# Kernel optimization log

Measured on AMD Instinct MI355X. Metric: run time of the kernel, lower is better.

The kernel has to match this reference:

```python
import jax, jax.numpy as jnp
import numpy as np

EPS = 1e-12
N_WAY, N_SHOT, C_IN, H_IN, W_IN = 5, 5, 640, 24, 24
TOP_LR = 0.8


def _normalize(x, axis):
    # torch F.normalize: x / max(||x||_2, eps)
    n = jnp.sqrt(jnp.sum(x * x, axis=axis, keepdims=True))
    return x / jnp.maximum(n, EPS)


def _conv1x1(x, W, b):
    # x: (B,C,H,W), W: (O,C), b: (O,)
    return jnp.einsum('bchw,oc->bohw', x, W) + b[None, :, None, None]


def _attlayer(x, Wc, bc, Wq, bq, Wk, bk):
    B, C, H, W = x.shape
    HW = H * W
    n_way, n_shot = N_WAY, N_SHOT
    scale = 1.0 / (C ** 0.5)
    x5 = _conv1x1(x, Wc, bc) + x
    x5 = _conv1x1(x5, Wq, bq)            # note: query_transform applied here
    # query_transform applied AGAIN (faithful to original)
    xq = _conv1x1(x5, Wq, bq).reshape(n_way, n_shot, C, HW)
    x_query = jnp.swapaxes(xq, 2, 3).reshape(n_way, n_shot * HW, C)
    xk = _conv1x1(x5, Wk, bk).reshape(n_way, n_shot, C, HW)
    x_key = jnp.swapaxes(xk, 1, 2).reshape(n_way, C, n_shot * HW)
    x_w1 = jnp.matmul(x_query, x_key) * scale          # (n_way, n_shot*HW, n_shot*HW)
    x_w = x_w1.reshape(n_way, n_shot * HW, n_shot, HW).max(-1).mean(-1)
    x_w = jax.nn.softmax(x_w.reshape(n_way, n_shot, HW), axis=-1)
    norm0 = _normalize(x5, 1).reshape(n_way, n_shot, C, H, W)
    # hard-max mask over spatial positions
    mask = (x_w == x_w.max(-1, keepdims=True)).astype(x.dtype)   # (n_way, n_shot, HW)
    seeds = (norm0 * mask.reshape(n_way, n_shot, 1, H, W)).sum((3, 4))  # (n_way, n_shot, C)
    # conv3d with 1x1 spatial kernel over full channel depth == einsum
    cor = jnp.einsum('nkcyx,okc->noyx', norm0, seeds).reshape(n_way, n_shot, HW)
    cmin = cor.min(-1, keepdims=True)
    cmax = cor.max(-1, keepdims=True)
    cor = (cor - cmin) / (cmax - cmin + EPS)
    cormap = cor.reshape(n_way * n_shot, 1, H, W)
    x51 = (x5 * cormap).reshape(n_way, n_shot, C, H, W)
    return x51.mean((1, 3, 4))  # (n_way, C)


def _cdsnet(lf):
    B, C, H, W = lf.shape
    HW = H * W
    n_way, n_shot = N_WAY, N_SHOT
    lfn = _normalize(lf, 1)
    X = jnp.swapaxes(lfn.reshape(B, C, HW), 1, 2)          # (B, HW, C)
    intra = X.reshape(n_way, n_shot * HW, C)
    # d_intra: masked (1-eye) gram mean == (x_i . S_way - ||x_i||^2)/(n_shot*HW)
    S_way = intra.sum(1)                                    # (n_way, C)
    d_intra = (jnp.einsum('nic,nc->ni', intra, S_way) - (intra * intra).sum(-1)) / (n_shot * HW)
    # d_inter: block-diagonal (same-image) pairs masked out
    S_tot = X.sum((0, 1))                                   # (C,)
    S_img = X.sum(1)                                        # (B, C)
    d_inter = (jnp.einsum('bic,c->bi', X, S_tot) - jnp.einsum('bic,bc->bi', X, S_img)) / (B * HW)
    cds = jax.nn.sigmoid(d_intra.reshape(n_way, -1) / d_inter.reshape(n_way, -1))  # (n_way, n_shot*HW)
    k = int(n_shot * HW * TOP_LR)
    _, sel_idx = jax.lax.top_k(cds, k)
    sel = jnp.zeros((n_way, n_shot * HW), lf.dtype)
    sel = sel.at[jnp.arange(n_way)[:, None], sel_idx].set(1.0)
    pos_small = sel.reshape(n_way * n_shot, 1, H, W)
    slf = lf * pos_small                                    # select_local_features
    slf_n = jnp.swapaxes(_normalize(slf.reshape(B, C, HW), 1), 1, 2)
    slf_n = slf_n.reshape(n_way, n_shot, HW, C)
    m1 = slf_n.reshape(n_way, n_shot * HW, C).mean(1)       # (n_way, C)
    l_intra = jnp.matmul(m1, m1.T) * (1.0 - jnp.eye(n_way, dtype=lf.dtype))
    m2 = slf_n.mean(2)                                      # (n_way, n_shot, C)
    l_inter = jnp.einsum('nsc,ntc->nst', m2, m2) * (1.0 - jnp.eye(n_shot, dtype=lf.dtype))
    loss = jnp.exp(l_inter.mean() / l_intra.mean())
    pos_index = jnp.broadcast_to(pos_small, (B, C, H, W))
    neg_index = 1.0 - pos_index
    return loss, pos_index, neg_index


def setup_inputs() -> dict:
    key = jax.random.key(0)
    ks = jax.random.split(key, 7)
    C = C_IN
    s = N_WAY * N_SHOT
    scale = 1.0 / np.sqrt(C)
    lf = jax.random.normal(ks[0], (s, C, H_IN, W_IN), jnp.float32)
    Wc = jax.random.normal(ks[1], (C, C), jnp.float32) * scale
    bc = jax.random.normal(ks[2], (C,), jnp.float32) * 0.01
    Wq = jax.random.normal(ks[3], (C, C), jnp.float32) * scale
    bq = jax.random.normal(ks[4], (C,), jnp.float32) * 0.01
    Wk = jax.random.normal(ks[5], (C, C), jnp.float32) * scale
    bk = jax.random.normal(ks[6], (C,), jnp.float32) * 0.01
    return {'local_feature': lf, 'Wc': Wc, 'bc': bc, 'Wq': Wq, 'bq': bq, 'Wk': Wk, 'bk': bk}


def reference(local_feature, Wc, bc, Wq, bq, Wk, bk):
    s, c, h, w = local_feature.shape
    hw = h * w
    proto1 = _attlayer(local_feature, Wc, bc, Wq, bq, Wk, bk)   # (n_way, C)
    global_proto = jnp.broadcast_to(proto1[:, None, :], (N_WAY, N_SHOT, c)).reshape(s, c)
    gpa = global_proto[:, None, :]                               # (s, 1, C) -> broadcasts to (s, HW, C)
    contrastive_loss, pos_index, neg_index = _cdsnet(local_feature)
    pos_x = _normalize(jnp.swapaxes((local_feature * pos_index).reshape(s, c, hw), 1, 2), -1)
    neg_x = _normalize(jnp.swapaxes((local_feature * neg_index).reshape(s, c, hw), 1, 2), -1)
    pos_value = jnp.exp(pos_x * gpa).sum(-1).mean(-1).mean(-1)
    neg_value = jnp.exp(neg_x * gpa).sum(-1).mean(-1).mean(-1)
    ctc_loss = -jnp.log(pos_value / neg_value)
    return (contrastive_loss, ctc_loss, pos_index)
```

## Files before the change

kernel.cpp:

```cpp
#include <hip/hip_runtime.h>
#include <math.h>

#define NW 5
#define NS 5
#define BB 25
#define CD 640
#define HWD 576
#define NP 2880
#define KTOP 2304
#define EPSF 1e-12f

typedef __attribute__((ext_vector_type(8))) short short8;
typedef __attribute__((ext_vector_type(4))) float f32x4;

__device__ inline unsigned short f2bf(float x) {
    unsigned u = __float_as_uint(x);
    return (unsigned short)((u + 0x7fffu + ((u >> 16) & 1u)) >> 16);
}
__device__ inline float bf2f(unsigned short h) { return __uint_as_float(((unsigned)h) << 16); }

__device__ inline void gload_lds16(const void* g, void* l) {
    __builtin_amdgcn_global_load_lds(
        (const __attribute__((address_space(1))) unsigned int*)g,
        (__attribute__((address_space(3))) unsigned int*)l, 16, 0, 0);
}

__global__ __launch_bounds__(256) void gemm640(
    const float* __restrict__ A0, const float* __restrict__ B0,
    const float* __restrict__ add0, float* __restrict__ C0, int mode0,
    const float* __restrict__ A1, const float* __restrict__ B1,
    const float* __restrict__ add1, float* __restrict__ C1, int mode1)
{
    __shared__ __align__(16) float At[32][68];
    __shared__ __align__(16) float Bt[32][64];
    const float *A, *B, *add; float* C; int mode;
    if (blockIdx.z == 0) { A = A0; B = B0; add = add0; C = C0; mode = mode0; }
    else                 { A = A1; B = B1; add = add1; C = C1; mode = mode1; }
    const int o0 = blockIdx.y * 64, j0 = blockIdx.x * 64;
    const int t  = threadIdx.x;
    const int to = (t >> 4) * 4, tj = (t & 15) * 4;

    float acc[4][4];
#pragma unroll
    for (int r = 0; r < 4; ++r)
#pragma unroll
        for (int s = 0; s < 4; ++s) acc[r][s] = 0.f;

    for (int c0 = 0; c0 < CD; c0 += 32) {
        __syncthreads();
        {
            const int r = t >> 3, c8 = (t & 7) * 8;
            float4 b0 = *(const float4*)&B[(size_t)(c0+r)*CD + j0 + c8];
            float4 b1 = *(const float4*)&B[(size_t)(c0+r)*CD + j0 + c8 + 4];
            *(float4*)&Bt[r][c8]     = b0;
            *(float4*)&Bt[r][c8 + 4] = b1;
            if (mode == 0) {
                float4 a0 = *(const float4*)&A[(size_t)(c0+r)*CD + o0 + c8];
                float4 a1 = *(const float4*)&A[(size_t)(c0+r)*CD + o0 + c8 + 4];
                *(float4*)&At[r][c8]     = a0;
                *(float4*)&At[r][c8 + 4] = a1;
            } else {
                const int r2 = t >> 2, c82 = (t & 3) * 8;
                float4 a0 = *(const float4*)&A[(size_t)(o0+r2)*CD + c0 + c82];
                float4 a1 = *(const float4*)&A[(size_t)(o0+r2)*CD + c0 + c82 + 4];
                At[c82+0][r2] = a0.x; At[c82+1][r2] = a0.y;
                At[c82+2][r2] = a0.z; At[c82+3][r2] = a0.w;
                At[c82+4][r2] = a1.x; At[c82+5][r2] = a1.y;
                At[c82+6][r2] = a1.z; At[c82+7][r2] = a1.w;
            }
        }
        __syncthreads();
#pragma unroll
        for (int kk = 0; kk < 32; ++kk) {
            float4 av = *(const float4*)&At[kk][to];
            float4 bv = *(const float4*)&Bt[kk][tj];
            float aa[4] = {av.x, av.y, av.z, av.w};
            float bb[4] = {bv.x, bv.y, bv.z, bv.w};
#pragma unroll
            for (int r = 0; r < 4; ++r)
#pragma unroll
                for (int s = 0; s < 4; ++s)
                    acc[r][s] = fmaf(aa[r], bb[s], acc[r][s]);
        }
    }

#pragma unroll
    for (int r = 0; r < 4; ++r) {
        float4 v;
        v.x = acc[r][0]; v.y = acc[r][1]; v.z = acc[r][2]; v.w = acc[r][3];
        if (add != nullptr) {
            float4 ad = *(const float4*)&add[(size_t)(o0+to+r)*CD + j0 + tj];
            v.x += ad.x; v.y += ad.y; v.z += ad.z; v.w += ad.w;
        }
        *(float4*)&C[(size_t)(o0+to+r)*CD + j0 + tj] = v;
    }
}

__global__ void matvec640(const float* __restrict__ A, const float* __restrict__ x,
                          const float* __restrict__ b, float* __restrict__ y)
{
    const int t = threadIdx.x;
    const int o = blockIdx.x*64 + (t >> 2);
    const int cb = (t & 3) * 160;
    const float* ap = A + (size_t)o*CD + cb;
    float a = 0.f;
    for (int m = 0; m < 160; m += 4) {
        float4 v = *(const float4*)&ap[m];
        a = fmaf(v.x, x[cb+m],   a);
        a = fmaf(v.y, x[cb+m+1], a);
        a = fmaf(v.z, x[cb+m+2], a);
        a = fmaf(v.w, x[cb+m+3], a);
    }
    a += __shfl_xor(a, 1, 64); a += __shfl_xor(a, 2, 64);
    if ((t & 3) == 0) y[o] = a + b[o];
}

__global__ void biasvec_kernel(const float* __restrict__ Wq, const float* __restrict__ Wk,
                               const float* __restrict__ bq, const float* __restrict__ bk,
                               float* __restrict__ wqtbk, float* __restrict__ bqwk,
                               float* __restrict__ sbb)
{
    const int c = threadIdx.x;
    const int m0 = blockIdx.x * 160;
    float s1 = 0.f, s2 = 0.f;
    for (int m = m0; m < m0 + 160; ++m) {
        s1 = fmaf(Wq[(size_t)m*CD + c], bk[m], s1);
        s2 = fmaf(bq[m], Wk[(size_t)m*CD + c], s2);
    }
    atomicAdd(&wqtbk[c], s1);
    atomicAdd(&bqwk[c], s2);
    if (c == 0) {
        float s3 = 0.f;
        for (int m = m0; m < m0 + 160; ++m) s3 = fmaf(bq[m], bk[m], s3);
        atomicAdd(sbb, s3);
    }
}

__global__ void wsplit2(const float* __restrict__ Weff, const float* __restrict__ M2e,
                        unsigned short* __restrict__ WeH, unsigned short* __restrict__ WeL,
                        unsigned short* __restrict__ MeH, unsigned short* __restrict__ MeL)
{
    int blk = blockIdx.x;
    const float* S; unsigned short *H, *L;
    if (blk < 400) { S = Weff; H = WeH; L = WeL; }
    else           { S = M2e;  H = MeH; L = MeL; blk -= 400; }
    int i = blk*256 + threadIdx.x;
    float4 v = ((const float4*)S)[i];
    ushort4 h, l;
    h.x = f2bf(v.x); h.y = f2bf(v.y); h.z = f2bf(v.z); h.w = f2bf(v.w);
    l.x = f2bf(v.x - bf2f(h.x)); l.y = f2bf(v.y - bf2f(h.y));
    l.z = f2bf(v.z - bf2f(h.z)); l.w = f2bf(v.w - bf2f(h.w));
    ((ushort4*)H)[i] = h; ((ushort4*)L)[i] = l;
}

__global__ __launch_bounds__(256) void convert_t(const float* __restrict__ in,
        unsigned short* __restrict__ Oh, unsigned short* __restrict__ Ol)
{
    __shared__ float tile[64][65];
    const int b  = blockIdx.y;
    const int c0 = (blockIdx.x / 9) * 64;
    const int p0 = (blockIdx.x % 9) * 64;
    const int t  = threadIdx.x;
    const float* src = in + (size_t)b * CD * HWD;
#pragma unroll
    for (int it = 0; it < 4; ++it) {
        int cl = (t >> 4) + 16*it, pl = (t & 15) * 4;
        float4 v = *(const float4*)&src[(size_t)(c0+cl)*HWD + p0 + pl];
        tile[cl][pl] = v.x; tile[cl][pl+1] = v.y; tile[cl][pl+2] = v.z; tile[cl][pl+3] = v.w;
    }
    __syncthreads();
#pragma unroll
    for (int it = 0; it < 4; ++it) {
        int pl = (t >> 4) + 16*it, clb = (t & 15) * 4;
        ushort4 hv, lv;
        float x0 = tile[clb+0][pl], x1 = tile[clb+1][pl], x2 = tile[clb+2][pl], x3 = tile[clb+3][pl];
        hv.x = f2bf(x0); hv.y = f2bf(x1); hv.z = f2bf(x2); hv.w = f2bf(x3);
        lv.x = f2bf(x0 - bf2f(hv.x)); lv.y = f2bf(x1 - bf2f(hv.y));
        lv.z = f2bf(x2 - bf2f(hv.z)); lv.w = f2bf(x3 - bf2f(hv.w));
        size_t o = (size_t)(b*HWD + p0 + pl) * CD + c0 + clb;
        *(ushort4*)&Oh[o] = hv;
        *(ushort4*)&Ol[o] = lv;
    }
}

__global__ __launch_bounds__(256) void conv2x(
    const unsigned short* __restrict__ Ah_, const unsigned short* __restrict__ Al_,
    const unsigned short* __restrict__ WeH, const unsigned short* __restrict__ WeL,
    const unsigned short* __restrict__ MeH, const unsigned short* __restrict__ MeL,
    const float* __restrict__ beff, const float* __restrict__ wbias,
    unsigned short* __restrict__ x5h, unsigned short* __restrict__ x5l,
    unsigned short* __restrict__ wh,  unsigned short* __restrict__ wl)
{
    __shared__ __align__(16) unsigned short lds[14336];
    const int obx  = blockIdx.x;
    const int osel = (obx < 5);
    const int o0   = (osel ? obx : obx - 5) * 128;
    const unsigned short* Wh = osel ? WeH : MeH;
    const unsigned short* Wl = osel ? WeL : MeL;
    const float* bias = osel ? beff : wbias;
    unsigned short* Oh = osel ? x5h : wh;
    unsigned short* Ol = osel ? x5l : wl;
    const int row0 = blockIdx.y * 96;
    const int t    = threadIdx.x;
    const int w    = t >> 6, lane = t & 63;
    const int ihalf = (w & 1) * 48;
    const int jhalf = (w >> 1) * 64;

    f32x4 acc[3][4];
#pragma unroll
    for (int f = 0; f < 3; ++f)
#pragma unroll
        for (int g = 0; g < 4; ++g) acc[f][g] = (f32x4){0.f,0.f,0.f,0.f};

    const int rl = lane >> 2;
    const int cl = (lane & 3) * 8;

    for (int c0 = 0; c0 < CD; c0 += 32) {
#pragma unroll
        for (int e = 0; e < 7; ++e) {
            const int s = w*7 + e;
            const unsigned short* src;
            if (s < 6)        src = Ah_ + (size_t)(row0 + s*16      + rl)*CD + c0 + cl;
            else if (s < 12)  src = Al_ + (size_t)(row0 + (s-6)*16  + rl)*CD + c0 + cl;
            else if (s < 20)  src = Wh  + (size_t)(o0   + (s-12)*16 + rl)*CD + c0 + cl;
            else              src = Wl  + (size_t)(o0   + (s-20)*16 + rl)*CD + c0 + cl;
            gload_lds16(src, &lds[s*512]);
        }
        __syncthreads();

        const int chunk = (lane >> 4) * 8;
        short8 afh[3], afl[3];
#pragma unroll
        for (int f = 0; f < 3; ++f) {
            int row = ihalf + f*16 + (lane & 15);
            afh[f] = *(const short8*)&lds[row*32 + chunk];
            afl[f] = *(const short8*)&lds[3072 + row*32 + chunk];
        }
#pragma unroll
        for (int g = 0; g < 4; ++g) {
            int row = jhalf + g*16 + (lane & 15);
            short8 bfh = *(const short8*)&lds[6144  + row*32 + chunk];
            short8 bfl = *(const short8*)&lds[10240 + row*32 + chunk];
#pragma unroll
            for (int f = 0; f < 3; ++f) {
                acc[f][g] = __builtin_amdgcn_mfma_f32_16x16x32_bf16(afh[f], bfh, acc[f][g], 0, 0, 0);
                acc[f][g] = __builtin_amdgcn_mfma_f32_16x16x32_bf16(afh[f], bfl, acc[f][g], 0, 0, 0);
                acc[f][g] = __builtin_amdgcn_mfma_f32_16x16x32_bf16(afl[f], bfh, acc[f][g], 0, 0, 0);
            }
        }
        __syncthreads();
    }

#pragma unroll
    for (int g = 0; g < 4; ++g) {
        const int o = o0 + jhalf + g*16 + (lane & 15);
        const float bs = bias[o];
#pragma unroll
        for (int f = 0; f < 3; ++f) {
            const int rbase = row0 + ihalf + f*16 + (lane >> 4)*4;
#pragma unroll
            for (int r = 0; r < 4; ++r) {
                const size_t idx = (size_t)(rbase + r)*CD + o;
                float v = acc[f][g][r] + bs;
                unsigned short hi = f2bf(v);
                Oh[idx] = hi;
                Ol[idx] = f2bf(v - bf2f(hi));
            }
        }
    }
}

__global__ __launch_bounds__(256) void qk_mfma(
    const unsigned short* __restrict__ Qh, const unsigned short* __restrict__ Ql,
    const unsigned short* __restrict__ Kh, const unsigned short* __restrict__ Kl,
    const float* __restrict__ rvec, float* __restrict__ xwp)
{
    __shared__ __align__(16) unsigned short lds[18432];
    const int n    = blockIdx.z;
    const int i0   = blockIdx.x * 96;
    const int shot = blockIdx.y / 3;
    const int jt   = blockIdx.y % 3;
    const int t    = threadIdx.x;
    const int w    = t >> 6, lane = t & 63;
    const int ihalf = (w & 1) * 48;
    const int jhalf = (w >> 1) * 96;

    const size_t qbase = (size_t)(n*NP + i0) * CD;
    const size_t kbase = (size_t)(n*NP + shot*HWD + jt*192) * CD;

    f32x4 acc[3][6];
#pragma unroll
    for (int f = 0; f < 3; ++f)
#pragma unroll
        for (int g = 0; g < 6; ++g) acc[f][g] = (f32x4){0.f,0.f,0.f,0.f};

    const int rl = lane >> 2;
    const int cl = (lane & 3) * 8;

    for (int c0 = 0; c0 < CD; c0 += 32) {
#pragma unroll
        for (int e = 0; e < 9; ++e) {
            const int s = w*9 + e;
            const int r = s*16 + rl;
            const unsigned short* src;
            if (s < 6)        src = Qh + qbase + (size_t)r*CD        + c0 + cl;
            else if (s < 12)  src = Ql + qbase + (size_t)(r-96)*CD   + c0 + cl;
            else if (s < 24)  src = Kh + kbase + (size_t)(r-192)*CD  + c0 + cl;
            else              src = Kl + kbase + (size_t)(r-384)*CD  + c0 + cl;
            gload_lds16(src, &lds[s*512]);
        }
        __syncthreads();

        const int chunk = (lane >> 4) * 8;
        short8 afh[3], afl[3];
#pragma unroll
        for (int f = 0; f < 3; ++f) {
            int row = ihalf + f*16 + (lane & 15);
            afh[f] = *(const short8*)&lds[row*32 + chunk];
            afl[f] = *(const short8*)&lds[3072 + row*32 + chunk];
        }
#pragma unroll
        for (int g = 0; g < 6; ++g) {
            int row = jhalf + g*16 + (lane & 15);
            short8 bfh = *(const short8*)&lds[6144  + row*32 + chunk];
            short8 bfl = *(const short8*)&lds[12288 + row*32 + chunk];
#pragma unroll
            for (int f = 0; f < 3; ++f) {
                acc[f][g] = __builtin_amdgcn_mfma_f32_16x16x32_bf16(afh[f], bfh, acc[f][g], 0, 0, 0);
                acc[f][g] = __builtin_amdgcn_mfma_f32_16x16x32_bf16(afh[f], bfl, acc[f][g], 0, 0, 0);
                acc[f][g] = __builtin_amdgcn_mfma_f32_16x16x32_bf16(afl[f], bfh, acc[f][g], 0, 0, 0);
            }
        }
        __syncthreads();
    }

    float rv[6];
    {
        int jg0 = n*NP + shot*HWD + jt*192 + jhalf + (lane & 15);
#pragma unroll
        for (int g = 0; g < 6; ++g) rv[g] = rvec[jg0 + g*16];
    }
    float* smax = (float*)lds;
#pragma unroll
    for (int f = 0; f < 3; ++f) {
#pragma unroll
        for (int r = 0; r < 4; ++r) {
            float m = -INFINITY;
#pragma unroll
            for (int g = 0; g < 6; ++g) m = fmaxf(m, acc[f][g][r] + rv[g]);
#pragma unroll
            for (int off = 1; off < 16; off <<= 1) m = fmaxf(m, __shfl_xor(m, off, 64));
            if ((lane & 15) == 0) smax[(ihalf + f*16 + (lane >> 4)*4 + r)*2 + (w >> 1)] = m;
        }
    }
    __syncthreads();
    if (t < 96) {
        float m = fmaxf(smax[t*2], smax[t*2 + 1]);
        xwp[(((size_t)n*5 + shot)*3 + jt)*NP + i0 + t] = m;
    }
}

__global__ void argmax_seeds(const float* __restrict__ xwp,
        const unsigned short* __restrict__ Xh, const unsigned short* __restrict__ Xl,
        const float* __restrict__ invn5, float* __restrict__ seeds)
{
    const int b = blockIdx.x;
    const int n = b / NS, sq = b % NS;
    const int t = threadIdx.x;
    __shared__ float wv[9]; __shared__ int wi[9]; __shared__ int spix;
    if (t < 576) {
        const int i = sq * HWD + t;
        float v = 0.f;
#pragma unroll
        for (int s = 0; s < NS; ++s) {
            float m = -INFINITY;
#pragma unroll
            for (int tt = 0; tt < 3; ++tt)
                m = fmaxf(m, xwp[(((size_t)(n*NS+s))*3 + tt)*NP + i]);
            v += m;
        }
        int lane = t & 63, w = t >> 6;
        float bv = v; int bi = t;
        for (int off = 32; off; off >>= 1) {
            float ov = __shfl_down(bv, off, 64);
            int   oi = __shfl_down(bi, off, 64);
            if (ov > bv || (ov == bv && oi < bi)) { bv = ov; bi = oi; }
        }
        if (lane == 0) { wv[w] = bv; wi[w] = bi; }
    }
    __syncthreads();
    if (t == 0) {
        float best = wv[0]; int bidx = wi[0];
        for (int k = 1; k < 9; ++k)
            if (wv[k] > best || (wv[k] == best && wi[k] < bidx)) { best = wv[k]; bidx = wi[k]; }
        spix = bidx;
    }
    __syncthreads();
    const int row = b*HWD + spix;
    float v = bf2f(Xh[(size_t)row*CD + t]) + bf2f(Xl[(size_t)row*CD + t]);
    seeds[b*CD + t] = v * invn5[row];
}

__global__ __launch_bounds__(256) void norms_rvec_T(const unsigned short* __restrict__ Xh,
        const unsigned short* __restrict__ Xl, const float* __restrict__ bqwk,
        const float* __restrict__ sbb, float* __restrict__ invn, float* __restrict__ rvec)
{
    const int t = threadIdx.x;
    const int row = blockIdx.x*64 + (t >> 2);
    const int cb = (t & 3) * 160;
    const unsigned short* ph = Xh + (size_t)row*CD + cb;
    const unsigned short* pl = Xl + (size_t)row*CD + cb;
    const float* wv = bqwk + cb;
    float a = 0.f, d = 0.f;
    for (int c = 0; c < 160; c += 8) {
        short8 h8 = *(const short8*)&ph[c];
        short8 l8 = *(const short8*)&pl[c];
#pragma unroll
        for (int j = 0; j < 8; ++j) {
            float v = bf2f((unsigned short)h8[j]) + bf2f((unsigned short)l8[j]);
            a = fmaf(v, v, a);
            d = fmaf(v, wv[c+j], d);
        }
    }
    a += __shfl_xor(a, 1, 64); a += __shfl_xor(a, 2, 64);
    d += __shfl_xor(d, 1, 64); d += __shfl_xor(d, 2, 64);
    if ((t & 3) == 0) {
        invn[row] = 1.f / fmaxf(sqrtf(a), EPSF);
        rvec[row] = d + sbb[0];
    }
}

__global__ __launch_bounds__(256) void pixel_norms(const float* __restrict__ src, float* __restrict__ invn)
{
    const int b = blockIdx.y, t = threadIdx.x;
    const int p = blockIdx.x*64 + (t >> 2);
    const int cb = (t & 3) * 160;
    const float* sp = src + (size_t)b*CD*HWD + p + (size_t)cb*HWD;
    float a = 0.f;
    for (int c = 0; c < 160; ++c) { float v = sp[(size_t)c*HWD]; a = fmaf(v, v, a); }
    a += __shfl_xor(a, 1, 64); a += __shfl_xor(a, 2, 64);
    if ((t & 3) == 0) invn[b*HWD + p] = 1.f / fmaxf(sqrtf(a), EPSF);
}

__global__ __launch_bounds__(256) void cor_T(const unsigned short* __restrict__ Xh,
        const unsigned short* __restrict__ Xl, const float* __restrict__ invn5,
        const float* __restrict__ seeds, float* __restrict__ cor)
{
    const int b = blockIdx.y;
    const int n = b / NS, k = b % NS;
    const int t = threadIdx.x;
    const int p = blockIdx.x*64 + (t >> 2);
    const int row = b*HWD + p;
    const int cb = (t & 3) * 160;
    const unsigned short* ph = Xh + (size_t)row*CD + cb;
    const unsigned short* pl = Xl + (size_t)row*CD + cb;
    float a[5] = {0.f,0.f,0.f,0.f,0.f};
    for (int c = 0; c < 160; c += 8) {
        short8 h8 = *(const short8*)&ph[c];
        short8 l8 = *(const short8*)&pl[c];
#pragma unroll
        for (int j = 0; j < 8; ++j) {
            float v = bf2f((unsigned short)h8[j]) + bf2f((unsigned short)l8[j]);
#pragma unroll
            for (int o = 0; o < 5; ++o)
                a[o] = fmaf(v, seeds[(o*NS + k)*CD + cb + c + j], a[o]);
        }
    }
    float in1 = invn5[row];
#pragma unroll
    for (int o = 0; o < 5; ++o) {
        float s = a[o];
        s += __shfl_xor(s, 1, 64); s += __shfl_xor(s, 2, 64);
        if ((t & 3) == 0) atomicAdd(&cor[(n*5 + o)*HWD + p], in1 * s);
    }
}

__global__ __launch_bounds__(256) void proto1_nm(const unsigned short* __restrict__ Xh,
        const unsigned short* __restrict__ Xl, const float* __restrict__ cor,
        float* __restrict__ proto1)
{
    __shared__ float corb[NP];
    __shared__ float sacc[256];
    __shared__ float mnv[5], mxv[5];
    const int n = blockIdx.y;
    const int t = threadIdx.x;
    for (int j = t; j < NP; j += 256) corb[j] = cor[n*NP + j];
    __syncthreads();
    if (t < 320) {
        int o = t >> 6, lane = t & 63;
        float mn = INFINITY, mx = -INFINITY;
        for (int j = lane; j < HWD; j += 64) {
            float v = corb[o*HWD + j];
            mn = fminf(mn, v); mx = fmaxf(mx, v);
        }
        for (int off = 32; off; off >>= 1) {
            mn = fminf(mn, __shfl_xor(mn, off, 64));
            mx = fmaxf(mx, __shfl_xor(mx, off, 64));
        }
        if (lane == 0) { mnv[o] = mn; mxv[o] = mx; }
    }
    __syncthreads();
    for (int j = t; j < NP; j += 256) {
        int o = j / HWD;
        corb[j] = (corb[j] - mnv[o]) / (mxv[o] - mnv[o] + EPSF);
    }
    __syncthreads();
    const int c = blockIdx.x*64 + (t & 63);
    const int rc = t >> 6;
    float a = 0.f;
    for (int rr = rc*720; rr < rc*720 + 720; ++rr) {
        size_t row = (size_t)(n*NP + rr);
        float v = bf2f(Xh[row*CD + c]) + bf2f(Xl[row*CD + c]);
        a = fmaf(v, corb[rr], a);
    }
    sacc[t] = a;
    __syncthreads();
    if (t < 64) {
        float s = sacc[t] + sacc[t+64] + sacc[t+128] + sacc[t+192];
        proto1[n*CD + c] = s * (1.f / 2880.f);
    }
}

__global__ void masked_sum(const float* __restrict__ lf, const float* __restrict__ invn,
                           const float* __restrict__ mask, float* __restrict__ out)
{
    int b = blockIdx.y; int ct = blockIdx.x;
    int t = threadIdx.x; int pi = t & 63, cj = t >> 6;
    int c = ct * 4 + cj;
    const float* xp = lf + ((size_t)b * CD + c) * HWD;
    const float* ip = invn + b * HWD;
    float acc = 0.f;
    if (mask != nullptr) {
        const float* mp = mask + b * HWD;
        for (int p = pi; p < HWD; p += 64) acc = fmaf(xp[p], ip[p] * mp[p], acc);
    } else {
        for (int p = pi; p < HWD; p += 64) acc = fmaf(xp[p], ip[p], acc);
    }
    for (int off = 32; off; off >>= 1) acc += __shfl_down(acc, off, 64);
    if (pi == 0) out[b * CD + c] = acc;
}

__global__ void sway_stot(const float* __restrict__ S_img, float* __restrict__ S_way,
                          float* __restrict__ S_tot)
{
    int c = threadIdx.x;
    float tot = 0.f;
    for (int nn = 0; nn < NW; ++nn) {
        float w = 0.f;
        for (int s = 0; s < NS; ++s) w += S_img[(nn*NS+s)*CD + c];
        S_way[nn*CD + c] = w; tot += w;
    }
    S_tot[c] = tot;
}

__global__ __launch_bounds__(256) void cds_v2(const float* __restrict__ lf, const float* __restrict__ invn,
                           const float* __restrict__ S_way, const float* __restrict__ S_img,
                           const float* __restrict__ S_tot, float* __restrict__ cds)
{
    const int b = blockIdx.y, t = threadIdx.x;
    const int p = blockIdx.x*64 + (t >> 2);
    const int cb = (t & 3) * 160;
    const int n = b / NS;
    const float* xp = lf + (size_t)b*CD*HWD + p + (size_t)cb*HWD;
    const float* wv = S_way + n*CD + cb;
    const float* iv = S_img + b*CD + cb;
    const float* tv = S_tot + cb;
    float dw = 0.f, di = 0.f, dt = 0.f, sq = 0.f;
    for (int c = 0; c < 160; ++c) {
        float v = xp[(size_t)c*HWD];
        dw = fmaf(v, wv[c], dw);
        di = fmaf(v, iv[c], di);
        dt = fmaf(v, tv[c], dt);
        sq = fmaf(v, v, sq);
    }
    dw += __shfl_xor(dw,1,64); dw += __shfl_xor(dw,2,64);
    di += __shfl_xor(di,1,64); di += __shfl_xor(di,2,64);
    dt += __shfl_xor(dt,1,64); dt += __shfl_xor(dt,2,64);
    sq += __shfl_xor(sq,1,64); sq += __shfl_xor(sq,2,64);
    if ((t & 3) == 0) {
        float in1 = invn[b*HWD + p];
        float d_intra = (in1 * dw - in1 * in1 * sq) * (1.f / 2880.f);
        float d_inter = (in1 * dt - in1 * di) * (1.f / 14400.f);
        float r = d_intra / d_inter;
        cds[n * NP + (b % NS) * HWD + p] = 1.f / (1.f + expf(-r));
    }
}

__global__ void topk_kernel(const float* __restrict__ cds, float* __restrict__ sel)
{
    __shared__ unsigned int u[NP];
    __shared__ int hist[256];
    __shared__ int red[16];
    __shared__ int bcast;
    __shared__ unsigned sprefix;
    __shared__ int skk;
    __shared__ int scanbuf[576];
    const int n = blockIdx.x, t = threadIdx.x;
    for (int j = t; j < NP; j += 576) {
        unsigned int x = __float_as_uint(cds[n * NP + j]);
        u[j] = (x & 0x80000000u) ? ~x : (x | 0x80000000u);
    }
    if (t == 0) { skk = KTOP; sprefix = 0u; }
    __syncthreads();
    const int j0 = t * 5;
    for (int byte = 3; byte >= 0; --byte) {
        if (t < 256) hist[t] = 0;
        __syncthreads();
        const int sh = byte * 8;
        const unsigned pmask = (byte == 3) ? 0u : (0xFFFFFFFFu << (sh + 8));
        const unsigned pref = sprefix;
#pragma unroll
        for (int e = 0; e < 5; ++e) {
            unsigned v = u[j0+e];
            if ((v & pmask) == pref) atomicAdd(&hist[(v >> sh) & 255], 1);
        }
        __syncthreads();
        if (t == 0) {
            int kk = skk, acc = 0, b2;
            for (b2 = 255; b2 >= 0; --b2) { acc += hist[b2]; if (acc >= kk) break; }
            skk = kk - (acc - hist[b2]);
            sprefix = pref | ((unsigned)b2 << sh);
        }
        __syncthreads();
    }
    const unsigned int T = sprefix;
    int cg = 0, ce = 0;
#pragma unroll
    for (int e = 0; e < 5; ++e) {
        unsigned v = u[j0+e];
        if (v > T) cg++; else if (v == T) ce++;
    }
    const int lane = t & 63, w = t >> 6;
    int r1 = cg;
    for (int off = 32; off; off >>= 1) r1 += __shfl_down(r1, off, 64);
    if (lane == 0) red[w] = r1;
    __syncthreads();
    if (t == 0) { int s2 = 0; for (int q = 0; q < 9; ++q) s2 += red[q]; bcast = s2; }
    __syncthreads();
    const int need = KTOP - bcast;
    scanbuf[t] = ce;
    __syncthreads();
    for (int off = 1; off < 576; off <<= 1) {
        int v2 = (t >= off) ? scanbuf[t - off] : 0;
        __syncthreads();
        scanbuf[t] += v2;
        __syncthreads();
    }
    int excl = scanbuf[t] - ce;
    int eidx = 0;
#pragma unroll
    for (int e = 0; e < 5; ++e) {
        int j = j0 + e;
        unsigned v = u[j];
        float s = 0.f;
        if (v > T) s = 1.f;
        else if (v == T) { if (excl + eidx < need) s = 1.f; eidx++; }
        int sh2 = j / HWD;
        sel[(n*NS + sh2) * HWD + (j - sh2*HWD)] = s;
    }
}

__global__ __launch_bounds__(256) void ctc_v2(const float* __restrict__ lf, const float* __restrict__ invn,
                           const float* __restrict__ proto1, const float* __restrict__ sel,
                           float* __restrict__ scal)
{
    const int b = blockIdx.y, t = threadIdx.x;
    const int p = blockIdx.x*64 + (t >> 2);
    const int cb = (t & 3) * 160;
    const int n = b / NS;
    const float* xp = lf + (size_t)b*CD*HWD + p + (size_t)cb*HWD;
    const float* pr = proto1 + n*CD + cb;
    float in1 = invn[b*HWD + p];
    float acc = 0.f;
    for (int c = 0; c < 160; ++c) acc += expf(xp[(size_t)c*HWD] * in1 * pr[c]);
    acc += __shfl_xor(acc, 1, 64); acc += __shfl_xor(acc, 2, 64);
    float pv = 0.f, nv = 0.f;
    if ((t & 3) == 0) {
        float s = sel[b*HWD + p];
        pv = (s > 0.5f) ? acc : 640.f;
        nv = (s > 0.5f) ? 640.f : acc;
    }
    for (int off = 32; off >= 4; off >>= 1) {
        pv += __shfl_down(pv, off, 64);
        nv += __shfl_down(nv, off, 64);
    }
    if ((t & 63) == 0) { atomicAdd(&scal[0], pv); atomicAdd(&scal[1], nv); }
}

__global__ void closs_fin(const float* __restrict__ Sm, const float* __restrict__ scal,
                          float* __restrict__ out)
{
    if (blockIdx.x == 1) {
        if (threadIdx.x == 0) out[1] = -(logf(scal[0]) - logf(scal[1]));
        return;
    }
    int c = threadIdx.x;
    double A = 0.0, Bv = 0.0, Cv = 0.0;
    float tot = 0.f;
    for (int nn = 0; nn < NW; ++nn) {
        float ws = 0.f;
        for (int s = 0; s < NS; ++s) {
            float v = Sm[(nn*NS+s)*CD + c];
            ws += v; Cv += (double)v * v;
        }
        tot += ws; A += (double)ws * ws;
    }
    Bv = (double)tot * tot;
    int lane = c & 63, w = c >> 6;
    for (int off = 32; off; off >>= 1) {
        A  += __shfl_down(A,  off, 64);
        Bv += __shfl_down(Bv, off, 64);
        Cv += __shfl_down(Cv, off, 64);
    }
    __shared__ double sa[10], sb[10], sc[10];
    if (lane == 0) { sa[w] = A; sb[w] = Bv; sc[w] = Cv; }
    __syncthreads();
    if (c == 0) {
        double a = 0, b2 = 0, cc = 0;
        for (int q = 0; q < 10; ++q) { a += sa[q]; b2 += sb[q]; cc += sc[q]; }
        out[0] = (float)exp(5.0 * (a - cc) / (b2 - a));
    }
}

__global__ void posindex_kernel(const float* __restrict__ sel, float* __restrict__ out2)
{
    int idx = blockIdx.x * 256 + threadIdx.x;
    int row = idx / 144;
    int f4  = idx - row * 144;
    int b   = row / CD;
    const float* sp = sel + b * HWD + f4 * 4;
    float* op = out2 + (size_t)row * HWD + f4 * 4;
    float2 v0 = make_float2(sp[0], sp[1]);
    float2 v1 = make_float2(sp[2], sp[3]);
    *(float2*)op = v0; *(float2*)(op + 2) = v1;
}

__global__ void init_zero(float* __restrict__ cor, float* __restrict__ scal,
                          float* __restrict__ wqtbk, float* __restrict__ bqwk,
                          float* __restrict__ sbb)
{
    int i = blockIdx.x * 256 + threadIdx.x;
    if (i < BB * HWD) cor[i] = 0.f;
    if (i < 640) { wqtbk[i] = 0.f; bqwk[i] = 0.f; }
    if (i < 2) scal[i] = 0.f;
    if (i == 0) sbb[0] = 0.f;
}

extern "C" void kernel_launch(void* const* d_in, const int* in_sizes, int n_in,
                              void* d_out, int out_size, void* d_ws, size_t ws_size,
                              hipStream_t stream) {
    const float* lf = (const float*)d_in[0];
    const float* Wc = (const float*)d_in[1];
    const float* bc = (const float*)d_in[2];
    const float* Wq = (const float*)d_in[3];
    const float* bq = (const float*)d_in[4];
    const float* Wk = (const float*)d_in[5];
    const float* bk = (const float*)d_in[6];
    float* out = (float*)d_out;
    float* ws = (float*)d_ws;

    const size_t FEAT = 9216000;
    size_t off = 0;
    auto alloc = [&](size_t nf) { float* p = ws + off; off += (nf + 3) & ~(size_t)3; return p; };
    float* s0     = alloc(FEAT);
    float* s1     = alloc(FEAT);
    float* xwp    = alloc(216000);
    float* seeds  = alloc(16000);
    float* invn5  = alloc(14400);
    float* invnl  = alloc(14400);
    float* cor    = alloc(14400);
    float* proto1 = alloc(3200);
    float* S_img  = alloc(16000);
    float* S_way  = alloc(3200);
    float* S_tot  = alloc(640);
    float* cds    = alloc(14400);
    float* sel    = alloc(14400);
    float* Sm     = alloc(16000);
    float* scal   = alloc(8);
    float* wqtbk  = alloc(640);
    float* bqwk   = alloc(640);
    float* sbb    = alloc(4);
    float* rvec   = alloc(14400);
    float* beff   = alloc(640);
    float* wbias  = alloc(640);
    float* WeS    = alloc(409600);
    float* MeS    = alloc(409600);

    float* M2   = s1;
    float* Weff = s1 + 409600;
    float* M2e  = s1 + 819200;

    unsigned short* WeH = (unsigned short*)WeS; unsigned short* WeL = WeH + 409600;
    unsigned short* MeH = (unsigned short*)MeS; unsigned short* MeL = MeH + 409600;

    unsigned short* lfTh = (unsigned short*)(out + 2);
    unsigned short* lfTl = lfTh + FEAT;

    unsigned short* s0h = (unsigned short*)s0; unsigned short* s0l = s0h + FEAT;
    unsigned short* s1h = (unsigned short*)s1; unsigned short* s1l = s1h + FEAT;

    init_zero<<<57, 256, 0, stream>>>(cor, scal, wqtbk, bqwk, sbb);
    gemm640<<<dim3(10,10,2), 256, 0, stream>>>(Wq, Wk, nullptr, M2, 0,
                                               Wq, Wc, Wq,      Weff, 1);
    biasvec_kernel<<<4, 640, 0, stream>>>(Wq, Wk, bq, bk, wqtbk, bqwk, sbb);
    gemm640<<<dim3(10,10,1), 256, 0, stream>>>(M2, Weff, nullptr, M2e, 1,
                                               M2, Weff, nullptr, M2e, 1);
    matvec640<<<10, 256, 0, stream>>>(Wq, bc, bq, beff);
    matvec640<<<10, 256, 0, stream>>>(M2, beff, wqtbk, wbias);
    wsplit2<<<800, 256, 0, stream>>>(Weff, M2e, WeH, WeL, MeH, MeL);

    convert_t<<<dim3(90,25), 256, 0, stream>>>(lf, lfTh, lfTl);

    conv2x<<<dim3(10,150), 256, 0, stream>>>(lfTh, lfTl, WeH, WeL, MeH, MeL,
                                             beff, wbias, s0h, s0l, s1h, s1l);

    norms_rvec_T<<<225, 256, 0, stream>>>(s0h, s0l, bqwk, sbb, invn5, rvec);

    qk_mfma<<<dim3(30,15,5), 256, 0, stream>>>(s0h, s0l, s1h, s1l, rvec, xwp);

    pixel_norms<<<dim3(9,25), 256, 0, stream>>>(lf, invnl);
    argmax_seeds<<<25, 640, 0, stream>>>(xwp, s0h, s0l, invn5, seeds);
    cor_T<<<dim3(9,25), 256, 0, stream>>>(s0h, s0l, invn5, seeds, cor);
    proto1_nm<<<dim3(10,5), 256, 0, stream>>>(s0h, s0l, cor, proto1);

    masked_sum<<<dim3(160,25), 256, 0, stream>>>(lf, invnl, nullptr, S_img);
    sway_stot<<<1, 640, 0, stream>>>(S_img, S_way, S_tot);
    cds_v2<<<dim3(9,25), 256, 0, stream>>>(lf, invnl, S_way, S_img, S_tot, cds);
    topk_kernel<<<5, 576, 0, stream>>>(cds, sel);
    masked_sum<<<dim3(160,25), 256, 0, stream>>>(lf, invnl, sel, Sm);

    ctc_v2<<<dim3(9,25), 256, 0, stream>>>(lf, invnl, proto1, sel, scal);
    closs_fin<<<2, 640, 0, stream>>>(Sm, scal, out);

    posindex_kernel<<<9000, 256, 0, stream>>>(sel, out + 2);
}
```

Measured before the change: 771.3 us.

## Merge independent kernels into multi-role launches and fuse row norms into conv epilogue

Independent kernels are merged into fewer launches, each dispatching on block index: weight GEMMs, bias matvecs, input conversion and zeroing run together in one launch, and post-processing stages are grouped into four launches. The M2e GEMM now writes its bf16 hi/lo split directly, so the fp32 intermediate and a separate split pass are gone. Row sum-of-squares and the bias dot product are accumulated inside the conv epilogue with shuffles and atomics, which removes the separate norms pass over the bf16 features. The intent is to cut launch overhead and redundant memory traffic. In exchange, the conv epilogue gets extra work and atomics, and the merged launches mix block types with uneven cost.

```diff
diff --git a/kernel.cpp b/kernel.cpp
--- a/kernel.cpp
+++ b/kernel.cpp
@@ -25,18 +25,14 @@
         (__attribute__((address_space(3))) unsigned int*)l, 16, 0, 0);
 }
 
-__global__ __launch_bounds__(256) void gemm640(
-    const float* __restrict__ A0, const float* __restrict__ B0,
-    const float* __restrict__ add0, float* __restrict__ C0, int mode0,
-    const float* __restrict__ A1, const float* __restrict__ B1,
-    const float* __restrict__ add1, float* __restrict__ C1, int mode1)
-{
-    __shared__ __align__(16) float At[32][68];
-    __shared__ __align__(16) float Bt[32][64];
-    const float *A, *B, *add; float* C; int mode;
-    if (blockIdx.z == 0) { A = A0; B = B0; add = add0; C = C0; mode = mode0; }
-    else                 { A = A1; B = B1; add = add1; C = C1; mode = mode1; }
-    const int o0 = blockIdx.y * 64, j0 = blockIdx.x * 64;
+__device__ void dev_gemm640(const float* __restrict__ A, const float* __restrict__ B,
+                            const float* __restrict__ add, float* __restrict__ C,
+                            unsigned short* __restrict__ H, unsigned short* __restrict__ L,
+                            int mode, int bx, int by, char* smem)
+{
+    float (*At)[68] = (float(*)[68])smem;
+    float (*Bt)[64] = (float(*)[64])(smem + 8704);
+    const int o0 = by * 64, j0 = bx * 64;
     const int t  = threadIdx.x;
     const int to = (t >> 4) * 4, tj = (t & 15) * 4;
 
@@ -86,80 +82,32 @@
 
 #pragma unroll
     for (int r = 0; r < 4; ++r) {
-        float4 v;
-        v.x = acc[r][0]; v.y = acc[r][1]; v.z = acc[r][2]; v.w = acc[r][3];
+        float v[4] = {acc[r][0], acc[r][1], acc[r][2], acc[r][3]};
+        const size_t base = (size_t)(o0+to+r)*CD + j0 + tj;
         if (add != nullptr) {
-            float4 ad = *(const float4*)&add[(size_t)(o0+to+r)*CD + j0 + tj];
-            v.x += ad.x; v.y += ad.y; v.z += ad.z; v.w += ad.w;
-        }
-        *(float4*)&C[(size_t)(o0+to+r)*CD + j0 + tj] = v;
-    }
-}
-
-__global__ void matvec640(const float* __restrict__ A, const float* __restrict__ x,
-                          const float* __restrict__ b, float* __restrict__ y)
-{
-    const int t = threadIdx.x;
-    const int o = blockIdx.x*64 + (t >> 2);
-    const int cb = (t & 3) * 160;
-    const float* ap = A + (size_t)o*CD + cb;
-    float a = 0.f;
-    for (int m = 0; m < 160; m += 4) {
-        float4 v = *(const float4*)&ap[m];
-        a = fmaf(v.x, x[cb+m],   a);
-        a = fmaf(v.y, x[cb+m+1], a);
-        a = fmaf(v.z, x[cb+m+2], a);
-        a = fmaf(v.w, x[cb+m+3], a);
-    }
-    a += __shfl_xor(a, 1, 64); a += __shfl_xor(a, 2, 64);
-    if ((t & 3) == 0) y[o] = a + b[o];
-}
-
-__global__ void biasvec_kernel(const float* __restrict__ Wq, const float* __restrict__ Wk,
-                               const float* __restrict__ bq, const float* __restrict__ bk,
-                               float* __restrict__ wqtbk, float* __restrict__ bqwk,
-                               float* __restrict__ sbb)
-{
-    const int c = threadIdx.x;
-    const int m0 = blockIdx.x * 160;
-    float s1 = 0.f, s2 = 0.f;
-    for (int m = m0; m < m0 + 160; ++m) {
-        s1 = fmaf(Wq[(size_t)m*CD + c], bk[m], s1);
-        s2 = fmaf(bq[m], Wk[(size_t)m*CD + c], s2);
-    }
-    atomicAdd(&wqtbk[c], s1);
-    atomicAdd(&bqwk[c], s2);
-    if (c == 0) {
-        float s3 = 0.f;
-        for (int m = m0; m < m0 + 160; ++m) s3 = fmaf(bq[m], bk[m], s3);
-        atomicAdd(sbb, s3);
-    }
-}
-
-__global__ void wsplit2(const float* __restrict__ Weff, const float* __restrict__ M2e,
-                        unsigned short* __restrict__ WeH, unsigned short* __restrict__ WeL,
-                        unsigned short* __restrict__ MeH, unsigned short* __restrict__ MeL)
-{
-    int blk = blockIdx.x;
-    const float* S; unsigned short *H, *L;
-    if (blk < 400) { S = Weff; H = WeH; L = WeL; }
-    else           { S = M2e;  H = MeH; L = MeL; blk -= 400; }
-    int i = blk*256 + threadIdx.x;
-    float4 v = ((const float4*)S)[i];
-    ushort4 h, l;
-    h.x = f2bf(v.x); h.y = f2bf(v.y); h.z = f2bf(v.z); h.w = f2bf(v.w);
-    l.x = f2bf(v.x - bf2f(h.x)); l.y = f2bf(v.y - bf2f(h.y));
-    l.z = f2bf(v.z - bf2f(h.z)); l.w = f2bf(v.w - bf2f(h.w));
-    ((ushort4*)H)[i] = h; ((ushort4*)L)[i] = l;
-}
-
-__global__ __launch_bounds__(256) void convert_t(const float* __restrict__ in,
-        unsigned short* __restrict__ Oh, unsigned short* __restrict__ Ol)
-{
-    __shared__ float tile[64][65];
-    const int b  = blockIdx.y;
-    const int c0 = (blockIdx.x / 9) * 64;
-    const int p0 = (blockIdx.x % 9) * 64;
+            float4 ad = *(const float4*)&add[base];
+            v[0] += ad.x; v[1] += ad.y; v[2] += ad.z; v[3] += ad.w;
+        }
+        if (C != nullptr) {
+            float4 o4; o4.x = v[0]; o4.y = v[1]; o4.z = v[2]; o4.w = v[3];
+            *(float4*)&C[base] = o4;
+        }
+        if (H != nullptr) {
+            ushort4 h, l;
+            h.x = f2bf(v[0]); h.y = f2bf(v[1]); h.z = f2bf(v[2]); h.w = f2bf(v[3]);
+            l.x = f2bf(v[0] - bf2f(h.x)); l.y = f2bf(v[1] - bf2f(h.y));
+            l.z = f2bf(v[2] - bf2f(h.z)); l.w = f2bf(v[3] - bf2f(h.w));
+            *(ushort4*)&H[base] = h; *(ushort4*)&L[base] = l;
+        }
+    }
+}
+
+__device__ void dev_convert(const float* __restrict__ in, unsigned short* __restrict__ Oh,
+                            unsigned short* __restrict__ Ol, int b, int xidx, char* smem)
+{
+    float (*tile)[65] = (float(*)[65])smem;
+    const int c0 = (xidx / 9) * 64;
+    const int p0 = (xidx % 9) * 64;
     const int t  = threadIdx.x;
     const float* src = in + (size_t)b * CD * HWD;
 #pragma unroll
@@ -183,13 +131,104 @@
     }
 }
 
+__global__ __launch_bounds__(256) void prep_a(
+    const float* __restrict__ lf, const float* __restrict__ Wc,
+    const float* __restrict__ bc, const float* __restrict__ Wq,
+    const float* __restrict__ bq, const float* __restrict__ Wk,
+    const float* __restrict__ bk,
+    float* __restrict__ M2, float* __restrict__ Weff,
+    float* __restrict__ wqtbk, float* __restrict__ bqwk, float* __restrict__ beff,
+    float* __restrict__ sbb,
+    unsigned short* __restrict__ lfTh, unsigned short* __restrict__ lfTl,
+    float* __restrict__ cor, float* __restrict__ sumsq, float* __restrict__ rvsum,
+    float* __restrict__ proto1, float* __restrict__ scal)
+{
+    __shared__ __align__(16) char smem[16896];
+    const int blk = blockIdx.x;
+    const int t = threadIdx.x;
+    if (blk < 100) {
+        dev_gemm640(Wq, Wk, nullptr, M2, nullptr, nullptr, 0, blk % 10, blk / 10, smem);
+    } else if (blk < 200) {
+        int b2 = blk - 100;
+        dev_gemm640(Wq, Wc, Wq, Weff, nullptr, nullptr, 1, b2 % 10, b2 / 10, smem);
+    } else if (blk < 210) {
+        const int o = (blk - 200)*64 + (t >> 2);
+        const int m0 = (t & 3) * 160;
+        float s1 = 0.f, s2 = 0.f;
+        for (int m = m0; m < m0 + 160; ++m) {
+            s1 = fmaf(Wq[(size_t)m*CD + o], bk[m], s1);
+            s2 = fmaf(bq[m], Wk[(size_t)m*CD + o], s2);
+        }
+        s1 += __shfl_xor(s1, 1, 64); s1 += __shfl_xor(s1, 2, 64);
+        s2 += __shfl_xor(s2, 1, 64); s2 += __shfl_xor(s2, 2, 64);
+        if ((t & 3) == 0) { wqtbk[o] = s1; bqwk[o] = s2; }
+    } else if (blk < 220) {
+        const int o = (blk - 210)*64 + (t >> 2);
+        const int m0 = (t & 3) * 160;
+        const float* ap = Wq + (size_t)o*CD + m0;
+        float a = 0.f;
+        for (int m = 0; m < 160; ++m) a = fmaf(ap[m], bc[m0 + m], a);
+        a += __shfl_xor(a, 1, 64); a += __shfl_xor(a, 2, 64);
+        if ((t & 3) == 0) beff[o] = a + bq[o];
+    } else if (blk == 220) {
+        __shared__ float red[4];
+        float a = 0.f;
+        for (int m = t; m < CD; m += 256) a = fmaf(bq[m], bk[m], a);
+        for (int off2 = 32; off2; off2 >>= 1) a += __shfl_down(a, off2, 64);
+        if ((t & 63) == 0) red[t >> 6] = a;
+        __syncthreads();
+        if (t == 0) sbb[0] = red[0] + red[1] + red[2] + red[3];
+    } else if (blk < 2471) {
+        const int idx = blk - 221;
+        dev_convert(lf, lfTh, lfTl, idx / 90, idx % 90, smem);
+    } else {
+        const int i0 = (blk - 2471)*256 + t;
+        for (int i = i0; i < 14400; i += 8192) { cor[i] = 0.f; sumsq[i] = 0.f; rvsum[i] = 0.f; }
+        for (int i = i0; i < 3200; i += 8192) proto1[i] = 0.f;
+        if (i0 < 2) scal[i0] = 0.f;
+    }
+}
+
+__global__ __launch_bounds__(256) void prep_b(
+    const float* __restrict__ M2, const float* __restrict__ Weff,
+    const float* __restrict__ beff, const float* __restrict__ wqtbk,
+    unsigned short* __restrict__ WeH, unsigned short* __restrict__ WeL,
+    unsigned short* __restrict__ MeH, unsigned short* __restrict__ MeL,
+    float* __restrict__ wbias)
+{
+    __shared__ __align__(16) char smem[16896];
+    const int blk = blockIdx.x;
+    const int t = threadIdx.x;
+    if (blk < 100) {
+        dev_gemm640(M2, Weff, nullptr, nullptr, MeH, MeL, 1, blk % 10, blk / 10, smem);
+    } else if (blk < 200) {
+        int i = (blk - 100)*256 + t;
+        float4 v = ((const float4*)Weff)[i];
+        ushort4 h, l;
+        h.x = f2bf(v.x); h.y = f2bf(v.y); h.z = f2bf(v.z); h.w = f2bf(v.w);
+        l.x = f2bf(v.x - bf2f(h.x)); l.y = f2bf(v.y - bf2f(h.y));
+        l.z = f2bf(v.z - bf2f(h.z)); l.w = f2bf(v.w - bf2f(h.w));
+        ((ushort4*)WeH)[i] = h; ((ushort4*)WeL)[i] = l;
+    } else {
+        const int o = (blk - 200)*64 + (t >> 2);
+        const int m0 = (t & 3) * 160;
+        const float* ap = M2 + (size_t)o*CD + m0;
+        float a = 0.f;
+        for (int m = 0; m < 160; ++m) a = fmaf(ap[m], beff[m0 + m], a);
+        a += __shfl_xor(a, 1, 64); a += __shfl_xor(a, 2, 64);
+        if ((t & 3) == 0) wbias[o] = a + wqtbk[o];
+    }
+}
+
 __global__ __launch_bounds__(256) void conv2x(
     const unsigned short* __restrict__ Ah_, const unsigned short* __restrict__ Al_,
     const unsigned short* __restrict__ WeH, const unsigned short* __restrict__ WeL,
     const unsigned short* __restrict__ MeH, const unsigned short* __restrict__ MeL,
     const float* __restrict__ beff, const float* __restrict__ wbias,
+    const float* __restrict__ bqwk,
     unsigned short* __restrict__ x5h, unsigned short* __restrict__ x5l,
-    unsigned short* __restrict__ wh,  unsigned short* __restrict__ wl)
+    unsigned short* __restrict__ wh,  unsigned short* __restrict__ wl,
+    float* __restrict__ sumsq, float* __restrict__ rvsum)
 {
     __shared__ __align__(16) unsigned short lds[14336];
     const int obx  = blockIdx.x;
@@ -251,20 +290,39 @@
         __syncthreads();
     }
 
+    float bs[4], bw[4];
 #pragma unroll
     for (int g = 0; g < 4; ++g) {
         const int o = o0 + jhalf + g*16 + (lane & 15);
-        const float bs = bias[o];
-#pragma unroll
-        for (int f = 0; f < 3; ++f) {
-            const int rbase = row0 + ihalf + f*16 + (lane >> 4)*4;
-#pragma unroll
-            for (int r = 0; r < 4; ++r) {
+        bs[g] = bias[o];
+        bw[g] = osel ? bqwk[o] : 0.f;
+    }
+#pragma unroll
+    for (int f = 0; f < 3; ++f) {
+        const int rbase = row0 + ihalf + f*16 + (lane >> 4)*4;
+#pragma unroll
+        for (int r = 0; r < 4; ++r) {
+            float sq = 0.f, rv = 0.f;
+#pragma unroll
+            for (int g = 0; g < 4; ++g) {
+                const int o = o0 + jhalf + g*16 + (lane & 15);
                 const size_t idx = (size_t)(rbase + r)*CD + o;
-                float v = acc[f][g][r] + bs;
+                float v = acc[f][g][r] + bs[g];
                 unsigned short hi = f2bf(v);
                 Oh[idx] = hi;
                 Ol[idx] = f2bf(v - bf2f(hi));
+                sq = fmaf(v, v, sq);
+                rv = fmaf(v, bw[g], rv);
+            }
+            if (osel) {
+                sq += __shfl_xor(sq, 1, 64); rv += __shfl_xor(rv, 1, 64);
+                sq += __shfl_xor(sq, 2, 64); rv += __shfl_xor(rv, 2, 64);
+                sq += __shfl_xor(sq, 4, 64); rv += __shfl_xor(rv, 4, 64);
+                sq += __shfl_xor(sq, 8, 64); rv += __shfl_xor(rv, 8, 64);
+                if ((lane & 15) == 0) {
+                    atomicAdd(&sumsq[rbase + r], sq);
+                    atomicAdd(&rvsum[rbase + r], rv);
+                }
             }
         }
     }
@@ -273,7 +331,8 @@
 __global__ __launch_bounds__(256) void qk_mfma(
     const unsigned short* __restrict__ Qh, const unsigned short* __restrict__ Ql,
     const unsigned short* __restrict__ Kh, const unsigned short* __restrict__ Kl,
-    const float* __restrict__ rvec, float* __restrict__ xwp)
+    const float* __restrict__ rvsum, const float* __restrict__ sbb,
+    float* __restrict__ xwp)
 {
     __shared__ __align__(16) unsigned short lds[18432];
     const int n    = blockIdx.z;
@@ -334,11 +393,12 @@
         __syncthreads();
     }
 
+    const float sv = sbb[0];
     float rv[6];
     {
         int jg0 = n*NP + shot*HWD + jt*192 + jhalf + (lane & 15);
 #pragma unroll
-        for (int g = 0; g < 6; ++g) rv[g] = rvec[jg0 + g*16];
+        for (int g = 0; g < 6; ++g) rv[g] = rvsum[jg0 + g*16] + sv;
     }
     float* smax = (float*)lds;
 #pragma unroll
@@ -360,13 +420,27 @@
     }
 }
 
-__global__ void argmax_seeds(const float* __restrict__ xwp,
-        const unsigned short* __restrict__ Xh, const unsigned short* __restrict__ Xl,
-        const float* __restrict__ invn5, float* __restrict__ seeds)
-{
-    const int b = blockIdx.x;
+__global__ __launch_bounds__(640) void post_a(
+    const float* __restrict__ lf, const float* __restrict__ xwp,
+    const unsigned short* __restrict__ Xh, const unsigned short* __restrict__ Xl,
+    const float* __restrict__ sumsq, float* __restrict__ invnl,
+    float* __restrict__ seeds)
+{
+    const int blk = blockIdx.x;
+    const int t = threadIdx.x;
+    if (blk < 90) {
+        const int pg = blk*160 + (t >> 2);
+        const int cb = (t & 3) * 160;
+        const int b = pg / HWD, p = pg - (pg / HWD) * HWD;
+        const float* sp = lf + (size_t)b*CD*HWD + (size_t)cb*HWD + p;
+        float a = 0.f;
+        for (int c = 0; c < 160; ++c) { float v = sp[(size_t)c*HWD]; a = fmaf(v, v, a); }
+        a += __shfl_xor(a, 1, 64); a += __shfl_xor(a, 2, 64);
+        if ((t & 3) == 0) invnl[pg] = 1.f / fmaxf(sqrtf(a), EPSF);
+        return;
+    }
+    const int b = blk - 90;
     const int n = b / NS, sq = b % NS;
-    const int t = threadIdx.x;
     __shared__ float wv[9]; __shared__ int wi[9]; __shared__ int spix;
     if (t < 576) {
         const int i = sq * HWD + t;
@@ -397,160 +471,123 @@
     }
     __syncthreads();
     const int row = b*HWD + spix;
+    const float in1 = 1.f / fmaxf(sqrtf(sumsq[row]), EPSF);
     float v = bf2f(Xh[(size_t)row*CD + t]) + bf2f(Xl[(size_t)row*CD + t]);
-    seeds[b*CD + t] = v * invn5[row];
-}
-
-__global__ __launch_bounds__(256) void norms_rvec_T(const unsigned short* __restrict__ Xh,
-        const unsigned short* __restrict__ Xl, const float* __restrict__ bqwk,
-        const float* __restrict__ sbb, float* __restrict__ invn, float* __restrict__ rvec)
-{
+    seeds[b*CD + t] = v * in1;
+}
+
+__global__ __launch_bounds__(256) void post_b(
+    const unsigned short* __restrict__ Xh, const unsigned short* __restrict__ Xl,
+    const float* __restrict__ sumsq, const float* __restrict__ seeds,
+    const float* __restrict__ lf, const float* __restrict__ invnl,
+    float* __restrict__ cor, float* __restrict__ S_img)
+{
+    const int blk = blockIdx.x;
     const int t = threadIdx.x;
-    const int row = blockIdx.x*64 + (t >> 2);
-    const int cb = (t & 3) * 160;
-    const unsigned short* ph = Xh + (size_t)row*CD + cb;
-    const unsigned short* pl = Xl + (size_t)row*CD + cb;
-    const float* wv = bqwk + cb;
-    float a = 0.f, d = 0.f;
-    for (int c = 0; c < 160; c += 8) {
-        short8 h8 = *(const short8*)&ph[c];
-        short8 l8 = *(const short8*)&pl[c];
-#pragma unroll
-        for (int j = 0; j < 8; ++j) {
-            float v = bf2f((unsigned short)h8[j]) + bf2f((unsigned short)l8[j]);
-            a = fmaf(v, v, a);
-            d = fmaf(v, wv[c+j], d);
-        }
-    }
-    a += __shfl_xor(a, 1, 64); a += __shfl_xor(a, 2, 64);
-    d += __shfl_xor(d, 1, 64); d += __shfl_xor(d, 2, 64);
-    if ((t & 3) == 0) {
-        invn[row] = 1.f / fmaxf(sqrtf(a), EPSF);
-        rvec[row] = d + sbb[0];
-    }
-}
-
-__global__ __launch_bounds__(256) void pixel_norms(const float* __restrict__ src, float* __restrict__ invn)
-{
-    const int b = blockIdx.y, t = threadIdx.x;
-    const int p = blockIdx.x*64 + (t >> 2);
-    const int cb = (t & 3) * 160;
-    const float* sp = src + (size_t)b*CD*HWD + p + (size_t)cb*HWD;
-    float a = 0.f;
-    for (int c = 0; c < 160; ++c) { float v = sp[(size_t)c*HWD]; a = fmaf(v, v, a); }
-    a += __shfl_xor(a, 1, 64); a += __shfl_xor(a, 2, 64);
-    if ((t & 3) == 0) invn[b*HWD + p] = 1.f / fmaxf(sqrtf(a), EPSF);
-}
-
-__global__ __launch_bounds__(256) void cor_T(const unsigned short* __restrict__ Xh,
-        const unsigned short* __restrict__ Xl, const float* __restrict__ invn5,
-        const float* __restrict__ seeds, float* __restrict__ cor)
-{
-    const int b = blockIdx.y;
-    const int n = b / NS, k = b % NS;
+    if (blk < 900) {
+        const int zc = blk / 225, rem = blk % 225;
+        const int pb = rem % 9, b = rem / 9;
+        const int n = b / NS, k = b % NS;
+        const int p = pb*64 + (t >> 2);
+        const int row = b*HWD + p;
+        const int cb = zc*160 + (t & 3) * 40;
+        const unsigned short* ph = Xh + (size_t)row*CD + cb;
+        const unsigned short* pl = Xl + (size_t)row*CD + cb;
+        float a[5] = {0.f,0.f,0.f,0.f,0.f};
+        for (int c = 0; c < 40; c += 8) {
+            short8 h8 = *(const short8*)&ph[c];
+            short8 l8 = *(const short8*)&pl[c];
+#pragma unroll
+            for (int j = 0; j < 8; ++j) {
+                float v = bf2f((unsigned short)h8[j]) + bf2f((unsigned short)l8[j]);
+#pragma unroll
+                for (int o = 0; o < 5; ++o)
+                    a[o] = fmaf(v, seeds[(o*NS + k)*CD + cb + c + j], a[o]);
+            }
+        }
+        const float in1 = 1.f / fmaxf(sqrtf(sumsq[row]), EPSF);
+#pragma unroll
+        for (int o = 0; o < 5; ++o) {
+            float s = a[o];
+            s += __shfl_xor(s, 1, 64); s += __shfl_xor(s, 2, 64);
+            if ((t & 3) == 0) atomicAdd(&cor[(n*5 + o)*HWD + p], in1 * s);
+        }
+        return;
+    }
+    const int i = blk - 900;
+    const int ct = i % 160, b = i / 160;
+    const int pi = t & 63, cj = t >> 6;
+    const int c = ct * 4 + cj;
+    const float* xp = lf + ((size_t)b * CD + c) * HWD;
+    const float* ip = invnl + b * HWD;
+    float acc = 0.f;
+    for (int p = pi; p < HWD; p += 64) acc = fmaf(xp[p], ip[p], acc);
+    for (int off = 32; off; off >>= 1) acc += __shfl_down(acc, off, 64);
+    if (pi == 0) S_img[b * CD + c] = acc;
+}
+
+__global__ __launch_bounds__(256) void post_c(
+    const unsigned short* __restrict__ Xh, const unsigned short* __restrict__ Xl,
+    const float* __restrict__ cor, const float* __restrict__ S_img,
+    float* __restrict__ proto1, float* __restrict__ S_way, float* __restrict__ S_tot)
+{
+    const int blk = blockIdx.x;
     const int t = threadIdx.x;
-    const int p = blockIdx.x*64 + (t >> 2);
-    const int row = b*HWD + p;
-    const int cb = (t & 3) * 160;
-    const unsigned short* ph = Xh + (size_t)row*CD + cb;
-    const unsigned short* pl = Xl + (size_t)row*CD + cb;
-    float a[5] = {0.f,0.f,0.f,0.f,0.f};
-    for (int c = 0; c < 160; c += 8) {
-        short8 h8 = *(const short8*)&ph[c];
-        short8 l8 = *(const short8*)&pl[c];
-#pragma unroll
-        for (int j = 0; j < 8; ++j) {
-            float v = bf2f((unsigned short)h8[j]) + bf2f((unsigned short)l8[j]);
-#pragma unroll
-            for (int o = 0; o < 5; ++o)
-                a[o] = fmaf(v, seeds[(o*NS + k)*CD + cb + c + j], a[o]);
-        }
-    }
-    float in1 = invn5[row];
-#pragma unroll
-    for (int o = 0; o < 5; ++o) {
-        float s = a[o];
-        s += __shfl_xor(s, 1, 64); s += __shfl_xor(s, 2, 64);
-        if ((t & 3) == 0) atomicAdd(&cor[(n*5 + o)*HWD + p], in1 * s);
-    }
-}
-
-__global__ __launch_bounds__(256) void proto1_nm(const unsigned short* __restrict__ Xh,
-        const unsigned short* __restrict__ Xl, const float* __restrict__ cor,
-        float* __restrict__ proto1)
-{
-    __shared__ float corb[NP];
-    __shared__ float sacc[256];
-    __shared__ float mnv[5], mxv[5];
-    const int n = blockIdx.y;
-    const int t = threadIdx.x;
-    for (int j = t; j < NP; j += 256) corb[j] = cor[n*NP + j];
-    __syncthreads();
-    if (t < 320) {
-        int o = t >> 6, lane = t & 63;
-        float mn = INFINITY, mx = -INFINITY;
-        for (int j = lane; j < HWD; j += 64) {
-            float v = corb[o*HWD + j];
-            mn = fminf(mn, v); mx = fmaxf(mx, v);
-        }
-        for (int off = 32; off; off >>= 1) {
-            mn = fminf(mn, __shfl_xor(mn, off, 64));
-            mx = fmaxf(mx, __shfl_xor(mx, off, 64));
-        }
-        if (lane == 0) { mnv[o] = mn; mxv[o] = mx; }
-    }
-    __syncthreads();
-    for (int j = t; j < NP; j += 256) {
-        int o = j / HWD;
-        corb[j] = (corb[j] - mnv[o]) / (mxv[o] - mnv[o] + EPSF);
-    }
-    __syncthreads();
-    const int c = blockIdx.x*64 + (t & 63);
-    const int rc = t >> 6;
-    float a = 0.f;
-    for (int rr = rc*720; rr < rc*720 + 720; ++rr) {
-        size_t row = (size_t)(n*NP + rr);
-        float v = bf2f(Xh[row*CD + c]) + bf2f(Xl[row*CD + c]);
-        a = fmaf(v, corb[rr], a);
-    }
-    sacc[t] = a;
-    __syncthreads();
-    if (t < 64) {
-        float s = sacc[t] + sacc[t+64] + sacc[t+128] + sacc[t+192];
-        proto1[n*CD + c] = s * (1.f / 2880.f);
-    }
-}
-
-__global__ void masked_sum(const float* __restrict__ lf, const float* __restrict__ invn,
-                           const float* __restrict__ mask, float* __restrict__ out)
-{
-    int b = blockIdx.y; int ct = blockIdx.x;
-    int t = threadIdx.x; int pi = t & 63, cj = t >> 6;
-    int c = ct * 4 + cj;
-    const float* xp = lf + ((size_t)b * CD + c) * HWD;
-    const float* ip = invn + b * HWD;
-    float acc = 0.f;
-    if (mask != nullptr) {
-        const float* mp = mask + b * HWD;
-        for (int p = pi; p < HWD; p += 64) acc = fmaf(xp[p], ip[p] * mp[p], acc);
-    } else {
-        for (int p = pi; p < HWD; p += 64) acc = fmaf(xp[p], ip[p], acc);
-    }
-    for (int off = 32; off; off >>= 1) acc += __shfl_down(acc, off, 64);
-    if (pi == 0) out[b * CD + c] = acc;
-}
-
-__global__ void sway_stot(const float* __restrict__ S_img, float* __restrict__ S_way,
-                          float* __restrict__ S_tot)
-{
-    int c = threadIdx.x;
-    float tot = 0.f;
-    for (int nn = 0; nn < NW; ++nn) {
-        float w = 0.f;
-        for (int s = 0; s < NS; ++s) w += S_img[(nn*NS+s)*CD + c];
-        S_way[nn*CD + c] = w; tot += w;
-    }
-    S_tot[c] = tot;
+    if (blk < 200) {
+        __shared__ float corb[NP];
+        __shared__ float sacc[256];
+        __shared__ float mnv[5], mxv[5];
+        const int n = blk / 40, rem = blk % 40;
+        const int ct = rem % 10, rch = rem / 10;
+        for (int j = t; j < NP; j += 256) corb[j] = cor[n*NP + j];
+        __syncthreads();
+        {
+            const int lane = t & 63;
+            for (int o = t >> 6; o < 5; o += 4) {
+                float mn = INFINITY, mx = -INFINITY;
+                for (int j = lane; j < HWD; j += 64) {
+                    float v = corb[o*HWD + j];
+                    mn = fminf(mn, v); mx = fmaxf(mx, v);
+                }
+                for (int off = 32; off; off >>= 1) {
+                    mn = fminf(mn, __shfl_xor(mn, off, 64));
+                    mx = fmaxf(mx, __shfl_xor(mx, off, 64));
+                }
+                if (lane == 0) { mnv[o] = mn; mxv[o] = mx; }
+            }
+        }
+        __syncthreads();
+        for (int j = t; j < NP; j += 256) {
+            int o = j / HWD;
+            corb[j] = (corb[j] - mnv[o]) / (mxv[o] - mnv[o] + EPSF);
+        }
+        __syncthreads();
+        const int c = ct*64 + (t & 63);
+        const int rc = t >> 6;
+        const int r0 = rch*720 + rc*180;
+        float a = 0.f;
+        for (int rr = r0; rr < r0 + 180; ++rr) {
+            size_t row = (size_t)(n*NP + rr);
+            float v = bf2f(Xh[row*CD + c]) + bf2f(Xl[row*CD + c]);
+            a = fmaf(v, corb[rr], a);
+        }
+        sacc[t] = a;
+        __syncthreads();
+        if (t < 64) {
+            float s = sacc[t] + sacc[t+64] + sacc[t+128] + sacc[t+192];
+            atomicAdd(&proto1[n*CD + c], s * (1.f / 2880.f));
+        }
+        return;
+    }
+    for (int c = t; c < CD; c += 256) {
+        float tot = 0.f;
+        for (int nn = 0; nn < NW; ++nn) {
+            float w = 0.f;
+            for (int s = 0; s < NS; ++s) w += S_img[(nn*NS+s)*CD + c];
+            S_way[nn*CD + c] = w; tot += w;
+        }
+        S_tot[c] = tot;
+    }
 }
 
 __global__ __launch_bounds__(256) void cds_v2(const float* __restrict__ lf, const float* __restrict__ invn,
@@ -660,17 +697,34 @@
     }
 }
 
-__global__ __launch_bounds__(256) void ctc_v2(const float* __restrict__ lf, const float* __restrict__ invn,
-                           const float* __restrict__ proto1, const float* __restrict__ sel,
-                           float* __restrict__ scal)
-{
-    const int b = blockIdx.y, t = threadIdx.x;
-    const int p = blockIdx.x*64 + (t >> 2);
+__global__ __launch_bounds__(256) void post_d(
+    const float* __restrict__ lf, const float* __restrict__ invnl,
+    const float* __restrict__ sel, const float* __restrict__ proto1,
+    float* __restrict__ Sm, float* __restrict__ scal)
+{
+    const int blk = blockIdx.x;
+    const int t = threadIdx.x;
+    if (blk < 4000) {
+        const int ct = blk % 160, b = blk / 160;
+        const int pi = t & 63, cj = t >> 6;
+        const int c = ct * 4 + cj;
+        const float* xp = lf + ((size_t)b * CD + c) * HWD;
+        const float* ip = invnl + b * HWD;
+        const float* mp = sel + b * HWD;
+        float acc = 0.f;
+        for (int p = pi; p < HWD; p += 64) acc = fmaf(xp[p], ip[p] * mp[p], acc);
+        for (int off = 32; off; off >>= 1) acc += __shfl_down(acc, off, 64);
+        if (pi == 0) Sm[b * CD + c] = acc;
+        return;
+    }
+    const int i = blk - 4000;
+    const int pb = i % 9, b = i / 9;
+    const int p = pb*64 + (t >> 2);
     const int cb = (t & 3) * 160;
     const int n = b / NS;
     const float* xp = lf + (size_t)b*CD*HWD + p + (size_t)cb*HWD;
     const float* pr = proto1 + n*CD + cb;
-    float in1 = invn[b*HWD + p];
+    float in1 = invnl[b*HWD + p];
     float acc = 0.f;
     for (int c = 0; c < 160; ++c) acc += expf(xp[(size_t)c*HWD] * in1 * pr[c]);
     acc += __shfl_xor(acc, 1, 64); acc += __shfl_xor(acc, 2, 64);
@@ -687,63 +741,55 @@
     if ((t & 63) == 0) { atomicAdd(&scal[0], pv); atomicAdd(&scal[1], nv); }
 }
 
-__global__ void closs_fin(const float* __restrict__ Sm, const float* __restrict__ scal,
-                          float* __restrict__ out)
-{
-    if (blockIdx.x == 1) {
-        if (threadIdx.x == 0) out[1] = -(logf(scal[0]) - logf(scal[1]));
+__global__ __launch_bounds__(256) void fin_kernel(
+    const float* __restrict__ sel, const float* __restrict__ Sm,
+    const float* __restrict__ scal, float* __restrict__ out)
+{
+    const int blk = blockIdx.x;
+    const int t = threadIdx.x;
+    if (blk < 9000) {
+        int idx = blk * 256 + t;
+        int row = idx / 144;
+        int f4  = idx - row * 144;
+        int b   = row / CD;
+        const float* sp = sel + b * HWD + f4 * 4;
+        float* op = out + 2 + (size_t)row * HWD + f4 * 4;
+        float2 v0 = make_float2(sp[0], sp[1]);
+        float2 v1 = make_float2(sp[2], sp[3]);
+        *(float2*)op = v0; *(float2*)(op + 2) = v1;
         return;
     }
-    int c = threadIdx.x;
+    if (blk == 9001) {
+        if (t == 0) out[1] = -(logf(scal[0]) - logf(scal[1]));
+        return;
+    }
+    __shared__ double sa[4], sb2[4], sc[4];
     double A = 0.0, Bv = 0.0, Cv = 0.0;
-    float tot = 0.f;
-    for (int nn = 0; nn < NW; ++nn) {
-        float ws = 0.f;
-        for (int s = 0; s < NS; ++s) {
-            float v = Sm[(nn*NS+s)*CD + c];
-            ws += v; Cv += (double)v * v;
-        }
-        tot += ws; A += (double)ws * ws;
-    }
-    Bv = (double)tot * tot;
-    int lane = c & 63, w = c >> 6;
+    for (int c = t; c < CD; c += 256) {
+        float tot = 0.f;
+        for (int nn = 0; nn < NW; ++nn) {
+            float ws = 0.f;
+            for (int s = 0; s < NS; ++s) {
+                float v = Sm[(nn*NS+s)*CD + c];
+                ws += v; Cv += (double)v * v;
+            }
+            tot += ws; A += (double)ws * ws;
+        }
+        Bv += (double)tot * tot;
+    }
+    const int lane = t & 63, w = t >> 6;
     for (int off = 32; off; off >>= 1) {
         A  += __shfl_down(A,  off, 64);
         Bv += __shfl_down(Bv, off, 64);
         Cv += __shfl_down(Cv, off, 64);
     }
-    __shared__ double sa[10], sb[10], sc[10];
-    if (lane == 0) { sa[w] = A; sb[w] = Bv; sc[w] = Cv; }
+    if (lane == 0) { sa[w] = A; sb2[w] = Bv; sc[w] = Cv; }
     __syncthreads();
-    if (c == 0) {
+    if (t == 0) {
         double a = 0, b2 = 0, cc = 0;
-        for (int q = 0; q < 10; ++q) { a += sa[q]; b2 += sb[q]; cc += sc[q]; }
+        for (int q = 0; q < 4; ++q) { a += sa[q]; b2 += sb2[q]; cc += sc[q]; }
         out[0] = (float)exp(5.0 * (a - cc) / (b2 - a));
     }
-}
-
-__global__ void posindex_kernel(const float* __restrict__ sel, float* __restrict__ out2)
-{
-    int idx = blockIdx.x * 256 + threadIdx.x;
-    int row = idx / 144;
-    int f4  = idx - row * 144;
-    int b   = row / CD;
-    const float* sp = sel + b * HWD + f4 * 4;
-    float* op = out2 + (size_t)row * HWD + f4 * 4;
-    float2 v0 = make_float2(sp[0], sp[1]);
-    float2 v1 = make_float2(sp[2], sp[3]);
-    *(float2*)op = v0; *(float2*)(op + 2) = v1;
-}
-
-__global__ void init_zero(float* __restrict__ cor, float* __restrict__ scal,
-                          float* __restrict__ wqtbk, float* __restrict__ bqwk,
-                          float* __restrict__ sbb)
-{
-    int i = blockIdx.x * 256 + threadIdx.x;
-    if (i < BB * HWD) cor[i] = 0.f;
-    if (i < 640) { wqtbk[i] = 0.f; bqwk[i] = 0.f; }
-    if (i < 2) scal[i] = 0.f;
-    if (i == 0) sbb[0] = 0.f;
 }
 
 extern "C" void kernel_launch(void* const* d_in, const int* in_sizes, int n_in,
@@ -766,8 +812,9 @@
     float* s1     = alloc(FEAT);
     float* xwp    = alloc(216000);
     float* seeds  = alloc(16000);
-    float* invn5  = alloc(14400);
     float* invnl  = alloc(14400);
+    float* sumsq  = alloc(14400);
+    float* rvsum  = alloc(14400);
     float* cor    = alloc(14400);
     float* proto1 = alloc(3200);
     float* S_img  = alloc(16000);
@@ -780,7 +827,6 @@
     float* wqtbk  = alloc(640);
     float* bqwk   = alloc(640);
     float* sbb    = alloc(4);
-    float* rvec   = alloc(14400);
     float* beff   = alloc(640);
     float* wbias  = alloc(640);
     float* WeS    = alloc(409600);
@@ -788,7 +834,6 @@
 
     float* M2   = s1;
     float* Weff = s1 + 409600;
-    float* M2e  = s1 + 819200;
 
     unsigned short* WeH = (unsigned short*)WeS; unsigned short* WeL = WeH + 409600;
     unsigned short* MeH = (unsigned short*)MeS; unsigned short* MeL = MeH + 409600;
@@ -799,38 +844,19 @@
     unsigned short* s0h = (unsigned short*)s0; unsigned short* s0l = s0h + FEAT;
     unsigned short* s1h = (unsigned short*)s1; unsigned short* s1l = s1h + FEAT;
 
-    init_zero<<<57, 256, 0, stream>>>(cor, scal, wqtbk, bqwk, sbb);
-    gemm640<<<dim3(10,10,2), 256, 0, stream>>>(Wq, Wk, nullptr, M2, 0,
-                                               Wq, Wc, Wq,      Weff, 1);
-    biasvec_kernel<<<4, 640, 0, stream>>>(Wq, Wk, bq, bk, wqtbk, bqwk, sbb);
-    gemm640<<<dim3(10,10,1), 256, 0, stream>>>(M2, Weff, nullptr, M2e, 1,
-                                               M2, Weff, nullptr, M2e, 1);
-    matvec640<<<10, 256, 0, stream>>>(Wq, bc, bq, beff);
-    matvec640<<<10, 256, 0, stream>>>(M2, beff, wqtbk, wbias);
-    wsplit2<<<800, 256, 0, stream>>>(Weff, M2e, WeH, WeL, MeH, MeL);
-
-    convert_t<<<dim3(90,25), 256, 0, stream>>>(lf, lfTh, lfTl);
-
+    prep_a<<<2503, 256, 0, stream>>>(lf, Wc, bc, Wq, bq, Wk, bk,
+                                     M2, Weff, wqtbk, bqwk, beff, sbb,
+                                     lfTh, lfTl, cor, sumsq, rvsum, proto1, scal);
+    prep_b<<<210, 256, 0, stream>>>(M2, Weff, beff, wqtbk, WeH, WeL, MeH, MeL, wbias);
     conv2x<<<dim3(10,150), 256, 0, stream>>>(lfTh, lfTl, WeH, WeL, MeH, MeL,
-                                             beff, wbias, s0h, s0l, s1h, s1l);
-
-    norms_rvec_T<<<225, 256, 0, stream>>>(s0h, s0l, bqwk, sbb, invn5, rvec);
-
-    qk_mfma<<<dim3(30,15,5), 256, 0, stream>>>(s0h, s0l, s1h, s1l, rvec, xwp);
-
-    pixel_norms<<<dim3(9,25), 256, 0, stream>>>(lf, invnl);
-    argmax_seeds<<<25, 640, 0, stream>>>(xwp, s0h, s0l, invn5, seeds);
-    cor_T<<<dim3(9,25), 256, 0, stream>>>(s0h, s0l, invn5, seeds, cor);
-    proto1_nm<<<dim3(10,5), 256, 0, stream>>>(s0h, s0l, cor, proto1);
-
-    masked_sum<<<dim3(160,25), 256, 0, stream>>>(lf, invnl, nullptr, S_img);
-    sway_stot<<<1, 640, 0, stream>>>(S_img, S_way, S_tot);
+                                             beff, wbias, bqwk,
+                                             s0h, s0l, s1h, s1l, sumsq, rvsum);
+    qk_mfma<<<dim3(30,15,5), 256, 0, stream>>>(s0h, s0l, s1h, s1l, rvsum, sbb, xwp);
+    post_a<<<115, 640, 0, stream>>>(lf, xwp, s0h, s0l, sumsq, invnl, seeds);
+    post_b<<<4900, 256, 0, stream>>>(s0h, s0l, sumsq, seeds, lf, invnl, cor, S_img);
+    post_c<<<201, 256, 0, stream>>>(s0h, s0l, cor, S_img, proto1, S_way, S_tot);
     cds_v2<<<dim3(9,25), 256, 0, stream>>>(lf, invnl, S_way, S_img, S_tot, cds);
     topk_kernel<<<5, 576, 0, stream>>>(cds, sel);
-    masked_sum<<<dim3(160,25), 256, 0, stream>>>(lf, invnl, sel, Sm);
-
-    ctc_v2<<<dim3(9,25), 256, 0, stream>>>(lf, invnl, proto1, sel, scal);
-    closs_fin<<<2, 640, 0, stream>>>(Sm, scal, out);
-
-    posindex_kernel<<<9000, 256, 0, stream>>>(sel, out + 2);
-}
+    post_d<<<4225, 256, 0, stream>>>(lf, invnl, sel, proto1, Sm, scal);
+    fin_kernel<<<9002, 256, 0, stream>>>(sel, Sm, scal, out);
+}
```

Result: faster. 709.3 us (-8.0%).
